# Kernel optimization log

Measured on AMD Instinct MI355X. Metric: run time of the kernel, lower is better.

## Reference

```python
import jax, jax.numpy as jnp
import numpy as np

E, K = 8, 2              # n_routed_experts, num_experts_per_tok
H, I = 2048, 1408        # hidden_size, moe_intermediate_size
IS = 2 * I               # shared experts intermediate (n_shared_experts * I)
B, S = 2, 512


def setup_inputs() -> dict:
    key = jax.random.key(0)
    ks = jax.random.split(key, 8)
    w = 0.02
    return {
        "hidden_states": jax.random.normal(ks[0], (B, S, H), jnp.float32),
        "router_w": jax.random.normal(ks[1], (E, H), jnp.float32) * w,
        "w_gate": jax.random.normal(ks[2], (E, I, H), jnp.float32) * w,
        "w_up": jax.random.normal(ks[3], (E, I, H), jnp.float32) * w,
        "w_down": jax.random.normal(ks[4], (E, H, I), jnp.float32) * w,
        "sw_gate": jax.random.normal(ks[5], (IS, H), jnp.float32) * w,
        "sw_up": jax.random.normal(ks[6], (IS, H), jnp.float32) * w,
        "sw_down": jax.random.normal(ks[7], (H, IS), jnp.float32) * w,
    }


def reference(hidden_states, router_w, w_gate, w_up, w_down, sw_gate, sw_up, sw_down):
    b, s, h = hidden_states.shape
    x = hidden_states.reshape(-1, h)                      # [T, H]
    t = x.shape[0]

    # Router: F.linear(x, gate_weight) -> softmax (fp32) -> topk (sorted)
    router_logits = x @ router_w.T                        # [T, E]
    scores = jax.nn.softmax(router_logits.astype(jnp.float32), axis=-1)
    routing_weights, selected = jax.lax.top_k(scores, K)  # [T, K]
    routing_weights = routing_weights / (routing_weights.sum(-1, keepdims=True) + 1e-6)
    routing_weights = routing_weights.astype(x.dtype)

    # Combine weights: [T, E], zero where expert not selected (exact gather/scatter math)
    cw = jnp.zeros((t, E), x.dtype).at[jnp.arange(t)[:, None], selected].add(routing_weights)

    # Per-expert SwiGLU FFN, batched over experts (grouped GEMM form)
    g = jnp.einsum('td,eid->eti', x, w_gate)              # [E, T, I]
    u = jnp.einsum('td,eid->eti', x, w_up)                # [E, T, I]
    y = jnp.einsum('eti,edi->etd', jax.nn.silu(g) * u, w_down)  # [E, T, H]
    moe_out = jnp.einsum('etd,te->td', y, cw)             # weighted combine -> [T, H]

    # Shared experts SwiGLU over all tokens
    shared = (jax.nn.silu(x @ sw_gate.T) * (x @ sw_up.T)) @ sw_down.T  # [T, H]

    final = (moe_out + shared).reshape(b, s, h)
    return final, router_logits
```

## Files before the change

### kernel.cpp

```cpp
#include <hip/hip_runtime.h>
#include <hip/hip_bf16.h>
#include <math.h>

#define T_TOK 1024
#define HDIM  2048
#define NEXP  8
#define IDIM  1408
#define ISH   2816
#define ROW_CAP 3072
#define ROWS_ALL 4096
#define MOE_TILES 24
#define NT_TOT 32

typedef __attribute__((ext_vector_type(8))) short bf16x8;
typedef __attribute__((ext_vector_type(4))) float f32x4;

static __device__ __forceinline__ unsigned short f2bf(float f) {
  __hip_bfloat16 h = __float2bfloat16(f);
  return __builtin_bit_cast(unsigned short, h);
}

__global__ __launch_bounds__(256) void router_kernel(
    const float* __restrict__ x, const float* __restrict__ rw,
    float* __restrict__ logits_out, int* __restrict__ selk, float* __restrict__ cwk)
{
  int t = blockIdx.x;
  int tid = threadIdx.x;
  float part[NEXP];
  const float* xr = x + (size_t)t * HDIM + tid * 8;
  float4 xa = *reinterpret_cast<const float4*>(xr);
  float4 xb = *reinterpret_cast<const float4*>(xr + 4);
  for (int e = 0; e < NEXP; ++e) {
    const float* wp = rw + (size_t)e * HDIM + tid * 8;
    float4 wa = *reinterpret_cast<const float4*>(wp);
    float4 wb = *reinterpret_cast<const float4*>(wp + 4);
    part[e] = xa.x*wa.x + xa.y*wa.y + xa.z*wa.z + xa.w*wa.w
            + xb.x*wb.x + xb.y*wb.y + xb.z*wb.z + xb.w*wb.w;
  }
  for (int e = 0; e < NEXP; ++e)
    for (int off = 32; off; off >>= 1)
      part[e] += __shfl_xor(part[e], off, 64);
  __shared__ float sums[4][NEXP];
  int wid = tid >> 6, lane = tid & 63;
  if (lane == 0) for (int e = 0; e < NEXP; ++e) sums[wid][e] = part[e];
  __syncthreads();
  if (tid == 0) {
    float lg[NEXP];
    for (int e = 0; e < NEXP; ++e) lg[e] = sums[0][e] + sums[1][e] + sums[2][e] + sums[3][e];
    float mx = lg[0];
    for (int e = 1; e < NEXP; ++e) mx = fmaxf(mx, lg[e]);
    float p[NEXP], s = 0.f;
    for (int e = 0; e < NEXP; ++e) { p[e] = expf(lg[e] - mx); s += p[e]; }
    for (int e = 0; e < NEXP; ++e) p[e] /= s;
    int i1 = 0;
    for (int e = 1; e < NEXP; ++e) if (lg[e] > lg[i1]) i1 = e;
    int i2 = -1;
    for (int e = 0; e < NEXP; ++e) { if (e == i1) continue; if (i2 < 0 || lg[e] > lg[i2]) i2 = e; }
    float denom = p[i1] + p[i2] + 1e-6f;
    selk[t*2] = i1; selk[t*2+1] = i2;
    cwk[t*2] = p[i1] / denom; cwk[t*2+1] = p[i2] / denom;
    for (int e = 0; e < NEXP; ++e) logits_out[t * NEXP + e] = lg[e];
  }
}

__global__ __launch_bounds__(512) void plan_kernel(
    const int* __restrict__ selk, const float* __restrict__ cwk,
    int* __restrict__ rowidx, int* __restrict__ tok_of_row,
    float* __restrict__ rowwgt, int* __restrict__ tile_tab)
{
  __shared__ int cnt[NEXP];
  __shared__ int seg[NEXP];
  int tid = threadIdx.x;
  int w = tid >> 6, lane = tid & 63;
  for (int i = tid; i < ROW_CAP; i += 512) { tok_of_row[i] = -1; rowwgt[i] = 0.f; }
  for (int i = tid; i < T_TOK; i += 512) { tok_of_row[ROW_CAP + i] = i; rowwgt[ROW_CAP + i] = 1.f; }
  int total = 0;
  for (int base = 0; base < 2 * T_TOK; base += 64) {
    unsigned long long m = __ballot(selk[base + lane] == w);
    total += __popcll(m);
  }
  if (lane == 0) cnt[w] = total;
  __syncthreads();
  if (tid == 0) {
    int s = 0;
    for (int e = 0; e < NEXP; ++e) { seg[e] = s; s += (cnt[e] + 127) & ~127; }
  }
  __syncthreads();
  int run = seg[w];
  for (int base = 0; base < 2 * T_TOK; base += 64) {
    int i = base + lane;
    bool f = selk[i] == w;
    unsigned long long m = __ballot(f);
    if (f) {
      int r = run + __popcll(m & ((1ull << lane) - 1ull));
      rowidx[i] = r;
      tok_of_row[r] = i >> 1;
      rowwgt[r] = cwk[i];
    }
    run += __popcll(m);
  }
  __syncthreads();
  if (tid < NT_TOT) {
    int e = -1, valid = 0;
    if (tid < MOE_TILES) {
      int base = tid * 128;
      for (int k = 0; k < NEXP; ++k) {
        int s0 = seg[k], s1 = s0 + ((cnt[k] + 127) & ~127);
        if (base >= s0 && base < s1) {
          e = k;
          valid = cnt[k] - (base - s0);
          if (valid > 128) valid = 128;
          if (valid < 0) valid = 0;
        }
      }
    } else { e = 0; valid = 128; }
    tile_tab[tid*2] = e;
    tile_tab[tid*2+1] = valid;
  }
}

__global__ __launch_bounds__(256) void gather_kernel(
    const float* __restrict__ x, const int* __restrict__ tok_of_row,
    unsigned short* __restrict__ xg)
{
  int r = blockIdx.x;
  int tid = threadIdx.x;
  int tok = tok_of_row[r];
  unsigned short* dst = xg + (size_t)r * HDIM + tid * 8;
  union { unsigned short us[8]; uint4 q; } p;
  if (tok < 0) {
    p.q = uint4{0, 0, 0, 0};
  } else {
    const float* src = x + (size_t)tok * HDIM + tid * 8;
    float4 a = *reinterpret_cast<const float4*>(src);
    float4 b = *reinterpret_cast<const float4*>(src + 4);
    p.us[0]=f2bf(a.x); p.us[1]=f2bf(a.y); p.us[2]=f2bf(a.z); p.us[3]=f2bf(a.w);
    p.us[4]=f2bf(b.x); p.us[5]=f2bf(b.y); p.us[6]=f2bf(b.z); p.us[7]=f2bf(b.w);
  }
  *reinterpret_cast<uint4*>(dst) = p.q;
}

static __device__ __forceinline__ void stage_b(
    const float* __restrict__ src, unsigned short (*Bs)[72], int brow, int bc)
{
  float4 v0 = *reinterpret_cast<const float4*>(src);
  float4 v1 = *reinterpret_cast<const float4*>(src + 4);
  float4 v2 = *reinterpret_cast<const float4*>(src + 8);
  float4 v3 = *reinterpret_cast<const float4*>(src + 12);
  union { unsigned short us[8]; uint4 q; } a, b;
  a.us[0]=f2bf(v0.x); a.us[1]=f2bf(v0.y); a.us[2]=f2bf(v0.z); a.us[3]=f2bf(v0.w);
  a.us[4]=f2bf(v1.x); a.us[5]=f2bf(v1.y); a.us[6]=f2bf(v1.z); a.us[7]=f2bf(v1.w);
  b.us[0]=f2bf(v2.x); b.us[1]=f2bf(v2.y); b.us[2]=f2bf(v2.z); b.us[3]=f2bf(v2.w);
  b.us[4]=f2bf(v3.x); b.us[5]=f2bf(v3.y); b.us[6]=f2bf(v3.z); b.us[7]=f2bf(v3.w);
  *reinterpret_cast<uint4*>(&Bs[brow][bc]) = a.q;
  *reinterpret_cast<uint4*>(&Bs[brow][bc + 8]) = b.q;
}

static __device__ __forceinline__ void stage_a(
    const unsigned short* __restrict__ abase, size_t lda, int k0,
    unsigned short* As, int wid, int lane)
{
  #pragma unroll
  for (int j = 0; j < 2; ++j) {
    int row = j * 64 + wid * 8 + (lane >> 3);
    int col = ((lane & 7) ^ (row & 7)) << 3;
    const unsigned short* src = abase + (size_t)row * lda + k0 + col;
    unsigned short* dst = &As[(j * 64 + wid * 8) * 64];
    __builtin_amdgcn_global_load_lds(
        (const __attribute__((address_space(1))) void*)src,
        (__attribute__((address_space(3))) void*)dst, 16, 0, 0);
  }
}

__global__ __launch_bounds__(512) void gu_kernel(
    const unsigned short* __restrict__ xg,
    const float* __restrict__ w_gate, const float* __restrict__ w_up,
    const float* __restrict__ sw_gate, const float* __restrict__ sw_up,
    const float* __restrict__ rowwgt, const int* __restrict__ tile_tab,
    unsigned short* __restrict__ hg, unsigned short* __restrict__ hsh)
{
  int mt = blockIdx.y, nt = blockIdx.x;
  int e = tile_tab[mt*2], valid = tile_tab[mt*2+1];
  bool sh = mt >= MOE_TILES;
  int ntiles = sh ? (ISH / 128) : (IDIM / 128);
  if (valid <= 0 || nt >= ntiles) return;
  int m0 = mt * 128, n0 = nt * 128;
  const float *wg, *wu; unsigned short* hout; int ldo;
  if (sh) { wg = sw_gate; wu = sw_up; hout = hsh + (size_t)(m0 - ROW_CAP) * ISH; ldo = ISH; }
  else {
    size_t wo = (size_t)e * IDIM * HDIM;
    wg = w_gate + wo; wu = w_up + wo;
    hout = hg + (size_t)m0 * IDIM; ldo = IDIM;
  }

  __shared__ unsigned short As[128 * 64];
  __shared__ unsigned short BgS[128][72];
  __shared__ unsigned short BuS[128][72];

  int tid = threadIdx.x, wid = tid >> 6, lane = tid & 63;
  int wr = wid >> 2, wc = wid & 3;
  int fr = lane & 15, fq8 = (lane >> 4) << 3;

  f32x4 accg[4][2] = {{}};
  f32x4 accu[4][2] = {{}};

  int brow = tid >> 2, bc = (tid & 3) << 4;
  const float* gsrc = wg + (size_t)(n0 + brow) * HDIM + bc;
  const float* usrc = wu + (size_t)(n0 + brow) * HDIM + bc;
  const unsigned short* abase = xg + (size_t)m0 * HDIM;

  for (int k0 = 0; k0 < HDIM; k0 += 64) {
    stage_a(abase, HDIM, k0, As, wid, lane);
    stage_b(gsrc + k0, BgS, brow, bc);
    stage_b(usrc + k0, BuS, brow, bc);
    __syncthreads();
    #pragma unroll
    for (int kk = 0; kk < 64; kk += 32) {
      bf16x8 a[4], bg[2], bu[2];
      #pragma unroll
      for (int m = 0; m < 4; ++m) {
        int row = wr * 64 + m * 16 + fr;
        a[m] = *reinterpret_cast<const bf16x8*>(&As[row * 64 + ((kk + fq8) ^ ((row & 7) << 3))]);
      }
      #pragma unroll
      for (int n = 0; n < 2; ++n) {
        bg[n] = *reinterpret_cast<const bf16x8*>(&BgS[wc * 32 + n * 16 + fr][kk + fq8]);
        bu[n] = *reinterpret_cast<const bf16x8*>(&BuS[wc * 32 + n * 16 + fr][kk + fq8]);
      }
      #pragma unroll
      for (int m = 0; m < 4; ++m)
        #pragma unroll
        for (int n = 0; n < 2; ++n) {
          accg[m][n] = __builtin_amdgcn_mfma_f32_16x16x32_bf16(a[m], bg[n], accg[m][n], 0, 0, 0);
          accu[m][n] = __builtin_amdgcn_mfma_f32_16x16x32_bf16(a[m], bu[n], accu[m][n], 0, 0, 0);
        }
    }
    __syncthreads();
  }
  int fq = lane >> 4;
  #pragma unroll
  for (int m = 0; m < 4; ++m)
    #pragma unroll
    for (int j = 0; j < 4; ++j) {
      int grow = wr * 64 + m * 16 + fq * 4 + j;
      float wv = rowwgt[m0 + grow];
      #pragma unroll
      for (int n = 0; n < 2; ++n) {
        float g = accg[m][n][j], u = accu[m][n][j];
        float hv = g / (1.f + __expf(-g)) * u * wv;
        hout[(size_t)grow * ldo + n0 + wc * 32 + n * 16 + fr] = f2bf(hv);
      }
    }
}

__global__ __launch_bounds__(512) void dn_kernel(
    const unsigned short* __restrict__ hg, const unsigned short* __restrict__ hsh,
    const float* __restrict__ w_down, const float* __restrict__ sw_down,
    const int* __restrict__ tile_tab,
    float* __restrict__ ydn, float* __restrict__ outf)
{
  int mt = blockIdx.y, nt = blockIdx.x;
  int e = tile_tab[mt*2], valid = tile_tab[mt*2+1];
  bool sh = mt >= MOE_TILES;
  if (valid <= 0) return;
  int m0 = mt * 128, n0 = nt * 128;
  const unsigned short* abase; const float* bbase; int K; float* obase;
  if (sh) { abase = hsh + (size_t)(m0 - ROW_CAP) * ISH; K = ISH; bbase = sw_down; obase = outf + (size_t)(m0 - ROW_CAP) * HDIM; }
  else { abase = hg + (size_t)m0 * IDIM; K = IDIM; bbase = w_down + (size_t)e * HDIM * IDIM; obase = ydn + (size_t)m0 * HDIM; }

  __shared__ unsigned short As[128 * 64];
  __shared__ unsigned short BsS[128][72];

  int tid = threadIdx.x, wid = tid >> 6, lane = tid & 63;
  int wr = wid >> 2, wc = wid & 3;
  int fr = lane & 15, fq8 = (lane >> 4) << 3;

  f32x4 acc[4][2] = {{}};

  int brow = tid >> 2, bc = (tid & 3) << 4;
  const float* bsrc = bbase + (size_t)(n0 + brow) * K + bc;

  for (int k0 = 0; k0 < K; k0 += 64) {
    stage_a(abase, K, k0, As, wid, lane);
    stage_b(bsrc + k0, BsS, brow, bc);
    __syncthreads();
    #pragma unroll
    for (int kk = 0; kk < 64; kk += 32) {
      bf16x8 a[4], b[2];
      #pragma unroll
      for (int m = 0; m < 4; ++m) {
        int row = wr * 64 + m * 16 + fr;
        a[m] = *reinterpret_cast<const bf16x8*>(&As[row * 64 + ((kk + fq8) ^ ((row & 7) << 3))]);
      }
      #pragma unroll
      for (int n = 0; n < 2; ++n)
        b[n] = *reinterpret_cast<const bf16x8*>(&BsS[wc * 32 + n * 16 + fr][kk + fq8]);
      #pragma unroll
      for (int m = 0; m < 4; ++m)
        #pragma unroll
        for (int n = 0; n < 2; ++n)
          acc[m][n] = __builtin_amdgcn_mfma_f32_16x16x32_bf16(a[m], b[n], acc[m][n], 0, 0, 0);
    }
    __syncthreads();
  }
  int fq = lane >> 4;
  #pragma unroll
  for (int m = 0; m < 4; ++m)
    #pragma unroll
    for (int j = 0; j < 4; ++j) {
      int grow = wr * 64 + m * 16 + fq * 4 + j;
      #pragma unroll
      for (int n = 0; n < 2; ++n)
        obase[(size_t)grow * HDIM + n0 + wc * 32 + n * 16 + fr] = acc[m][n][j];
    }
}

__global__ __launch_bounds__(256) void combine_kernel(
    const float* __restrict__ ydn, const int* __restrict__ rowidx,
    float* __restrict__ outf)
{
  int t = blockIdx.x;
  int c = threadIdx.x * 8;
  int r0 = rowidx[t*2], r1 = rowidx[t*2+1];
  const float4* a0 = reinterpret_cast<const float4*>(ydn + (size_t)r0 * HDIM + c);
  const float4* a1 = reinterpret_cast<const float4*>(ydn + (size_t)r1 * HDIM + c);
  float4* o = reinterpret_cast<float4*>(outf + (size_t)t * HDIM + c);
  float4 x0 = a0[0], x1 = a0[1], y0 = a1[0], y1 = a1[1];
  float4 o0 = o[0], o1 = o[1];
  o0.x += x0.x + y0.x; o0.y += x0.y + y0.y; o0.z += x0.z + y0.z; o0.w += x0.w + y0.w;
  o1.x += x1.x + y1.x; o1.y += x1.y + y1.y; o1.z += x1.z + y1.z; o1.w += x1.w + y1.w;
  o[0] = o0; o[1] = o1;
}

extern "C" void kernel_launch(void* const* d_in, const int* in_sizes, int n_in,
                              void* d_out, int out_size, void* d_ws, size_t ws_size,
                              hipStream_t stream) {
  const float* x      = (const float*)d_in[0];
  const float* rw     = (const float*)d_in[1];
  const float* w_gate = (const float*)d_in[2];
  const float* w_up   = (const float*)d_in[3];
  const float* w_down = (const float*)d_in[4];
  const float* sw_g   = (const float*)d_in[5];
  const float* sw_u   = (const float*)d_in[6];
  const float* sw_d   = (const float*)d_in[7];
  float* out_final  = (float*)d_out;
  float* out_logits = out_final + (size_t)T_TOK * HDIM;

  char* ws = (char*)d_ws;
  int*   selk     = (int*)(ws + 0);
  float* cwk      = (float*)(ws + 8192);
  int*   rowidx   = (int*)(ws + 16384);
  int*   tokrow   = (int*)(ws + 24576);
  float* rowwgt   = (float*)(ws + 40960);
  int*   tile_tab = (int*)(ws + 57344);
  unsigned short* xg  = (unsigned short*)(ws + 65536);
  unsigned short* hg  = (unsigned short*)(ws + 65536 + 16777216);
  unsigned short* hsh = (unsigned short*)(ws + 65536 + 16777216 + 8650752);
  float* ydn = (float*)(ws + 65536 + 16777216 + 8650752 + 5767168);

  router_kernel<<<T_TOK, 256, 0, stream>>>(x, rw, out_logits, selk, cwk);
  plan_kernel<<<1, 512, 0, stream>>>(selk, cwk, rowidx, tokrow, rowwgt, tile_tab);
  gather_kernel<<<ROWS_ALL, 256, 0, stream>>>(x, tokrow, xg);
  gu_kernel<<<dim3(ISH / 128, NT_TOT), 512, 0, stream>>>(
      xg, w_gate, w_up, sw_g, sw_u, rowwgt, tile_tab, hg, hsh);
  dn_kernel<<<dim3(HDIM / 128, NT_TOT), 512, 0, stream>>>(
      hg, hsh, w_down, sw_d, tile_tab, ydn, out_final);
  combine_kernel<<<T_TOK, 256, 0, stream>>>(ydn, rowidx, out_final);
}
```

Before: 276.5 us.

## Software-pipeline GEMM K-loop with double-buffered A and remap tile launch order

Both grouped GEMM kernels now prefetch the next K-slice: the A tile goes asynchronously into a second LDS buffer, and the fp32 weight slice is loaded into registers while the current slice's MFMAs run. The register copy is converted and written to LDS after a barrier. The 2D grid is replaced by a flat 1D grid with a custom block-to-tile mapping. This drops the dead blocks the old grid spent on MoE tiles with too few column tiles, and interleaves blocks across the XCDs so weight tiles are shared. The cost is more registers and LDS, and an extra barrier per iteration.

```diff
diff --git a/kernel.cpp b/kernel.cpp
--- a/kernel.cpp
+++ b/kernel.cpp
@@ -140,20 +140,24 @@
   *reinterpret_cast<uint4*>(dst) = p.q;
 }
 
-static __device__ __forceinline__ void stage_b(
-    const float* __restrict__ src, unsigned short (*Bs)[72], int brow, int bc)
-{
-  float4 v0 = *reinterpret_cast<const float4*>(src);
-  float4 v1 = *reinterpret_cast<const float4*>(src + 4);
-  float4 v2 = *reinterpret_cast<const float4*>(src + 8);
-  float4 v3 = *reinterpret_cast<const float4*>(src + 12);
+static __device__ __forceinline__ void bwrite(
+    unsigned short (*Bs)[72], int brow, int bc, const float4* v)
+{
   union { unsigned short us[8]; uint4 q; } a, b;
-  a.us[0]=f2bf(v0.x); a.us[1]=f2bf(v0.y); a.us[2]=f2bf(v0.z); a.us[3]=f2bf(v0.w);
-  a.us[4]=f2bf(v1.x); a.us[5]=f2bf(v1.y); a.us[6]=f2bf(v1.z); a.us[7]=f2bf(v1.w);
-  b.us[0]=f2bf(v2.x); b.us[1]=f2bf(v2.y); b.us[2]=f2bf(v2.z); b.us[3]=f2bf(v2.w);
-  b.us[4]=f2bf(v3.x); b.us[5]=f2bf(v3.y); b.us[6]=f2bf(v3.z); b.us[7]=f2bf(v3.w);
+  a.us[0]=f2bf(v[0].x); a.us[1]=f2bf(v[0].y); a.us[2]=f2bf(v[0].z); a.us[3]=f2bf(v[0].w);
+  a.us[4]=f2bf(v[1].x); a.us[5]=f2bf(v[1].y); a.us[6]=f2bf(v[1].z); a.us[7]=f2bf(v[1].w);
+  b.us[0]=f2bf(v[2].x); b.us[1]=f2bf(v[2].y); b.us[2]=f2bf(v[2].z); b.us[3]=f2bf(v[2].w);
+  b.us[4]=f2bf(v[3].x); b.us[5]=f2bf(v[3].y); b.us[6]=f2bf(v[3].z); b.us[7]=f2bf(v[3].w);
   *reinterpret_cast<uint4*>(&Bs[brow][bc]) = a.q;
   *reinterpret_cast<uint4*>(&Bs[brow][bc + 8]) = b.q;
+}
+
+static __device__ __forceinline__ void bload(const float* __restrict__ src, float4* v)
+{
+  v[0] = *reinterpret_cast<const float4*>(src);
+  v[1] = *reinterpret_cast<const float4*>(src + 4);
+  v[2] = *reinterpret_cast<const float4*>(src + 8);
+  v[3] = *reinterpret_cast<const float4*>(src + 12);
 }
 
 static __device__ __forceinline__ void stage_a(
@@ -179,11 +183,15 @@
     const float* __restrict__ rowwgt, const int* __restrict__ tile_tab,
     unsigned short* __restrict__ hg, unsigned short* __restrict__ hsh)
 {
-  int mt = blockIdx.y, nt = blockIdx.x;
+  int bid = blockIdx.x;
+  int lb = (bid & 7) * 55 + (bid >> 3);
+  int mt, nt;
+  if (lb < MOE_TILES * 11) { mt = lb % MOE_TILES; nt = lb / MOE_TILES; }
+  else { int s = lb - MOE_TILES * 11; mt = MOE_TILES + (s & 7); nt = s >> 3; }
+
   int e = tile_tab[mt*2], valid = tile_tab[mt*2+1];
+  if (valid <= 0) return;
   bool sh = mt >= MOE_TILES;
-  int ntiles = sh ? (ISH / 128) : (IDIM / 128);
-  if (valid <= 0 || nt >= ntiles) return;
   int m0 = mt * 128, n0 = nt * 128;
   const float *wg, *wu; unsigned short* hout; int ldo;
   if (sh) { wg = sw_gate; wu = sw_up; hout = hsh + (size_t)(m0 - ROW_CAP) * ISH; ldo = ISH; }
@@ -193,7 +201,7 @@
     hout = hg + (size_t)m0 * IDIM; ldo = IDIM;
   }
 
-  __shared__ unsigned short As[128 * 64];
+  __shared__ unsigned short As[2][128 * 64];
   __shared__ unsigned short BgS[128][72];
   __shared__ unsigned short BuS[128][72];
 
@@ -209,18 +217,26 @@
   const float* usrc = wu + (size_t)(n0 + brow) * HDIM + bc;
   const unsigned short* abase = xg + (size_t)m0 * HDIM;
 
-  for (int k0 = 0; k0 < HDIM; k0 += 64) {
-    stage_a(abase, HDIM, k0, As, wid, lane);
-    stage_b(gsrc + k0, BgS, brow, bc);
-    stage_b(usrc + k0, BuS, brow, bc);
-    __syncthreads();
+  float4 pg[4], pu[4];
+  bload(gsrc, pg); bload(usrc, pu);
+  stage_a(abase, HDIM, 0, As[0], wid, lane);
+  bwrite(BgS, brow, bc, pg);
+  bwrite(BuS, brow, bc, pu);
+  __syncthreads();
+
+  const int NK = HDIM / 64;
+  for (int t = 0; t < NK; ++t) {
+    int cur = t & 1;
+    int k1 = (t + 1 < NK) ? (t + 1) * 64 : 0;
+    bload(gsrc + k1, pg); bload(usrc + k1, pu);
+    stage_a(abase, HDIM, k1, As[cur ^ 1], wid, lane);
     #pragma unroll
     for (int kk = 0; kk < 64; kk += 32) {
       bf16x8 a[4], bg[2], bu[2];
       #pragma unroll
       for (int m = 0; m < 4; ++m) {
         int row = wr * 64 + m * 16 + fr;
-        a[m] = *reinterpret_cast<const bf16x8*>(&As[row * 64 + ((kk + fq8) ^ ((row & 7) << 3))]);
+        a[m] = *reinterpret_cast<const bf16x8*>(&As[cur][row * 64 + ((kk + fq8) ^ ((row & 7) << 3))]);
       }
       #pragma unroll
       for (int n = 0; n < 2; ++n) {
@@ -236,7 +252,11 @@
         }
     }
     __syncthreads();
-  }
+    bwrite(BgS, brow, bc, pg);
+    bwrite(BuS, brow, bc, pu);
+    __syncthreads();
+  }
+
   int fq = lane >> 4;
   #pragma unroll
   for (int m = 0; m < 4; ++m)
@@ -259,16 +279,21 @@
     const int* __restrict__ tile_tab,
     float* __restrict__ ydn, float* __restrict__ outf)
 {
-  int mt = blockIdx.y, nt = blockIdx.x;
+  int bid = blockIdx.x;
+  int lb = (bid & 7) * 64 + (bid >> 3);
+  int mt, nt;
+  if (lb < MOE_TILES * 16) { mt = lb % MOE_TILES; nt = lb / MOE_TILES; }
+  else { int s = lb - MOE_TILES * 16; mt = MOE_TILES + (s & 7); nt = s >> 3; }
+
   int e = tile_tab[mt*2], valid = tile_tab[mt*2+1];
+  if (valid <= 0) return;
   bool sh = mt >= MOE_TILES;
-  if (valid <= 0) return;
   int m0 = mt * 128, n0 = nt * 128;
   const unsigned short* abase; const float* bbase; int K; float* obase;
   if (sh) { abase = hsh + (size_t)(m0 - ROW_CAP) * ISH; K = ISH; bbase = sw_down; obase = outf + (size_t)(m0 - ROW_CAP) * HDIM; }
   else { abase = hg + (size_t)m0 * IDIM; K = IDIM; bbase = w_down + (size_t)e * HDIM * IDIM; obase = ydn + (size_t)m0 * HDIM; }
 
-  __shared__ unsigned short As[128 * 64];
+  __shared__ unsigned short As[2][128 * 64];
   __shared__ unsigned short BsS[128][72];
 
   int tid = threadIdx.x, wid = tid >> 6, lane = tid & 63;
@@ -280,17 +305,25 @@
   int brow = tid >> 2, bc = (tid & 3) << 4;
   const float* bsrc = bbase + (size_t)(n0 + brow) * K + bc;
 
-  for (int k0 = 0; k0 < K; k0 += 64) {
-    stage_a(abase, K, k0, As, wid, lane);
-    stage_b(bsrc + k0, BsS, brow, bc);
-    __syncthreads();
+  float4 pb[4];
+  bload(bsrc, pb);
+  stage_a(abase, K, 0, As[0], wid, lane);
+  bwrite(BsS, brow, bc, pb);
+  __syncthreads();
+
+  const int NK = K / 64;
+  for (int t = 0; t < NK; ++t) {
+    int cur = t & 1;
+    int k1 = (t + 1 < NK) ? (t + 1) * 64 : 0;
+    bload(bsrc + k1, pb);
+    stage_a(abase, K, k1, As[cur ^ 1], wid, lane);
     #pragma unroll
     for (int kk = 0; kk < 64; kk += 32) {
       bf16x8 a[4], b[2];
       #pragma unroll
       for (int m = 0; m < 4; ++m) {
         int row = wr * 64 + m * 16 + fr;
-        a[m] = *reinterpret_cast<const bf16x8*>(&As[row * 64 + ((kk + fq8) ^ ((row & 7) << 3))]);
+        a[m] = *reinterpret_cast<const bf16x8*>(&As[cur][row * 64 + ((kk + fq8) ^ ((row & 7) << 3))]);
       }
       #pragma unroll
       for (int n = 0; n < 2; ++n)
@@ -301,6 +334,8 @@
         for (int n = 0; n < 2; ++n)
           acc[m][n] = __builtin_amdgcn_mfma_f32_16x16x32_bf16(a[m], b[n], acc[m][n], 0, 0, 0);
     }
+    __syncthreads();
+    bwrite(BsS, brow, bc, pb);
     __syncthreads();
   }
   int fq = lane >> 4;
@@ -361,9 +396,9 @@
   router_kernel<<<T_TOK, 256, 0, stream>>>(x, rw, out_logits, selk, cwk);
   plan_kernel<<<1, 512, 0, stream>>>(selk, cwk, rowidx, tokrow, rowwgt, tile_tab);
   gather_kernel<<<ROWS_ALL, 256, 0, stream>>>(x, tokrow, xg);
-  gu_kernel<<<dim3(ISH / 128, NT_TOT), 512, 0, stream>>>(
+  gu_kernel<<<440, 512, 0, stream>>>(
       xg, w_gate, w_up, sw_g, sw_u, rowwgt, tile_tab, hg, hsh);
-  dn_kernel<<<dim3(HDIM / 128, NT_TOT), 512, 0, stream>>>(
+  dn_kernel<<<512, 512, 0, stream>>>(
       hg, hsh, w_down, sw_d, tile_tab, ydn, out_final);
   combine_kernel<<<T_TOK, 256, 0, stream>>>(ydn, rowidx, out_final);
 }
```

Result: slower. 338.8 us (+22.5%).

## Restructure MoE GEMMs into 128x32 tiles with triple-buffered A and register-direct B

Applied to the files above, without the earlier changes.

The gate/up and down GEMM kernels now use 128x32 output tiles with 256 threads. B weights are loaded straight from global fp32 into registers and converted to bf16 in-register, which drops the LDS staging for B. The A operand is triple-buffered in LDS via global_load_lds, and a vmcnt-based wait plus one barrier per step replaces the two __syncthreads. The 1D grid is remapped with an XCD-aware (bid&7) swizzle that groups tiles sharing weight columns. This aims to overlap loads with MFMA and raise parallelism, but each block re-reads A for fewer output columns and the hand-tuned vmcnt counts are fragile.

```diff
diff --git a/kernel.cpp b/kernel.cpp
--- a/kernel.cpp
+++ b/kernel.cpp
@@ -11,6 +11,7 @@
 #define ROWS_ALL 4096
 #define MOE_TILES 24
 #define NT_TOT 32
+#define ATILE (128*64)
 
 typedef __attribute__((ext_vector_type(8))) short bf16x8;
 typedef __attribute__((ext_vector_type(4))) float f32x4;
@@ -18,6 +19,13 @@
 static __device__ __forceinline__ unsigned short f2bf(float f) {
   __hip_bfloat16 h = __float2bfloat16(f);
   return __builtin_bit_cast(unsigned short, h);
+}
+
+static __device__ __forceinline__ bf16x8 cvt8(float4 a, float4 b) {
+  union { unsigned short us[8]; bf16x8 v; } r;
+  r.us[0]=f2bf(a.x); r.us[1]=f2bf(a.y); r.us[2]=f2bf(a.z); r.us[3]=f2bf(a.w);
+  r.us[4]=f2bf(b.x); r.us[5]=f2bf(b.y); r.us[6]=f2bf(b.z); r.us[7]=f2bf(b.w);
+  return r.v;
 }
 
 __global__ __launch_bounds__(256) void router_kernel(
@@ -140,51 +148,116 @@
   *reinterpret_cast<uint4*>(dst) = p.q;
 }
 
-static __device__ __forceinline__ void stage_b(
-    const float* __restrict__ src, unsigned short (*Bs)[72], int brow, int bc)
-{
-  float4 v0 = *reinterpret_cast<const float4*>(src);
-  float4 v1 = *reinterpret_cast<const float4*>(src + 4);
-  float4 v2 = *reinterpret_cast<const float4*>(src + 8);
-  float4 v3 = *reinterpret_cast<const float4*>(src + 12);
-  union { unsigned short us[8]; uint4 q; } a, b;
-  a.us[0]=f2bf(v0.x); a.us[1]=f2bf(v0.y); a.us[2]=f2bf(v0.z); a.us[3]=f2bf(v0.w);
-  a.us[4]=f2bf(v1.x); a.us[5]=f2bf(v1.y); a.us[6]=f2bf(v1.z); a.us[7]=f2bf(v1.w);
-  b.us[0]=f2bf(v2.x); b.us[1]=f2bf(v2.y); b.us[2]=f2bf(v2.z); b.us[3]=f2bf(v2.w);
-  b.us[4]=f2bf(v3.x); b.us[5]=f2bf(v3.y); b.us[6]=f2bf(v3.z); b.us[7]=f2bf(v3.w);
-  *reinterpret_cast<uint4*>(&Bs[brow][bc]) = a.q;
-  *reinterpret_cast<uint4*>(&Bs[brow][bc + 8]) = b.q;
-}
-
-static __device__ __forceinline__ void stage_a(
+static __device__ __forceinline__ void stage_a3(
     const unsigned short* __restrict__ abase, size_t lda, int k0,
     unsigned short* As, int wid, int lane)
 {
   #pragma unroll
-  for (int j = 0; j < 2; ++j) {
-    int row = j * 64 + wid * 8 + (lane >> 3);
+  for (int j = 0; j < 4; ++j) {
+    int row = j * 32 + wid * 8 + (lane >> 3);
     int col = ((lane & 7) ^ (row & 7)) << 3;
     const unsigned short* src = abase + (size_t)row * lda + k0 + col;
-    unsigned short* dst = &As[(j * 64 + wid * 8) * 64];
+    unsigned short* dst = &As[(j * 32 + wid * 8) * 64];
     __builtin_amdgcn_global_load_lds(
         (const __attribute__((address_space(1))) void*)src,
         (__attribute__((address_space(3))) void*)dst, 16, 0, 0);
   }
 }
 
-__global__ __launch_bounds__(512) void gu_kernel(
+struct BStage2 { float4 g0, g1, g2, g3, u0, u1, u2, u3; };
+struct BStage1 { float4 b0, b1, b2, b3; };
+
+static __device__ __forceinline__ void loadB2(
+    const float* __restrict__ pg, const float* __restrict__ pu, int k, BStage2& s)
+{
+  s.g0 = *reinterpret_cast<const float4*>(pg + k);
+  s.g1 = *reinterpret_cast<const float4*>(pg + k + 4);
+  s.g2 = *reinterpret_cast<const float4*>(pg + k + 32);
+  s.g3 = *reinterpret_cast<const float4*>(pg + k + 36);
+  s.u0 = *reinterpret_cast<const float4*>(pu + k);
+  s.u1 = *reinterpret_cast<const float4*>(pu + k + 4);
+  s.u2 = *reinterpret_cast<const float4*>(pu + k + 32);
+  s.u3 = *reinterpret_cast<const float4*>(pu + k + 36);
+}
+
+static __device__ __forceinline__ void loadB1(
+    const float* __restrict__ pb, int k, BStage1& s)
+{
+  s.b0 = *reinterpret_cast<const float4*>(pb + k);
+  s.b1 = *reinterpret_cast<const float4*>(pb + k + 4);
+  s.b2 = *reinterpret_cast<const float4*>(pb + k + 32);
+  s.b3 = *reinterpret_cast<const float4*>(pb + k + 36);
+}
+
+static __device__ __forceinline__ void stepGU(
+    const BStage2& s, const unsigned short* Abuf,
+    int wr, int fr, int fq8, f32x4* accg, f32x4* accu)
+{
+  bf16x8 bg0 = cvt8(s.g0, s.g1), bg1 = cvt8(s.g2, s.g3);
+  bf16x8 bu0 = cvt8(s.u0, s.u1), bu1 = cvt8(s.u2, s.u3);
+  #pragma unroll
+  for (int kk = 0; kk < 2; ++kk) {
+    bf16x8 a[4];
+    #pragma unroll
+    for (int m = 0; m < 4; ++m) {
+      int row = wr * 64 + m * 16 + fr;
+      a[m] = *reinterpret_cast<const bf16x8*>(
+          &Abuf[row * 64 + ((kk * 32 + fq8) ^ ((row & 7) << 3))]);
+    }
+    bf16x8 bg = kk ? bg1 : bg0;
+    bf16x8 bu = kk ? bu1 : bu0;
+    #pragma unroll
+    for (int m = 0; m < 4; ++m) {
+      accg[m] = __builtin_amdgcn_mfma_f32_16x16x32_bf16(a[m], bg, accg[m], 0, 0, 0);
+      accu[m] = __builtin_amdgcn_mfma_f32_16x16x32_bf16(a[m], bu, accu[m], 0, 0, 0);
+    }
+  }
+}
+
+static __device__ __forceinline__ void stepDN(
+    const BStage1& s, const unsigned short* Abuf,
+    int wr, int fr, int fq8, f32x4* acc)
+{
+  bf16x8 b0 = cvt8(s.b0, s.b1), b1 = cvt8(s.b2, s.b3);
+  #pragma unroll
+  for (int kk = 0; kk < 2; ++kk) {
+    bf16x8 a[4];
+    #pragma unroll
+    for (int m = 0; m < 4; ++m) {
+      int row = wr * 64 + m * 16 + fr;
+      a[m] = *reinterpret_cast<const bf16x8*>(
+          &Abuf[row * 64 + ((kk * 32 + fq8) ^ ((row & 7) << 3))]);
+    }
+    bf16x8 b = kk ? b1 : b0;
+    #pragma unroll
+    for (int m = 0; m < 4; ++m)
+      acc[m] = __builtin_amdgcn_mfma_f32_16x16x32_bf16(a[m], b, acc[m], 0, 0, 0);
+  }
+}
+
+#define WAIT_BARRIER(N) do { \
+    asm volatile("s_waitcnt vmcnt(" #N ")" ::: "memory"); \
+    __builtin_amdgcn_s_barrier(); \
+    __builtin_amdgcn_sched_barrier(0); \
+  } while (0)
+
+__global__ __launch_bounds__(256) void gu_kernel(
     const unsigned short* __restrict__ xg,
     const float* __restrict__ w_gate, const float* __restrict__ w_up,
     const float* __restrict__ sw_gate, const float* __restrict__ sw_up,
     const float* __restrict__ rowwgt, const int* __restrict__ tile_tab,
     unsigned short* __restrict__ hg, unsigned short* __restrict__ hsh)
 {
-  int mt = blockIdx.y, nt = blockIdx.x;
+  int bid = blockIdx.x;
+  int lb = (bid & 7) * 220 + (bid >> 3);
+  int mt, nt;
+  if (lb < MOE_TILES * 44) { mt = lb % MOE_TILES; nt = lb / MOE_TILES; }
+  else { int s = lb - MOE_TILES * 44; mt = MOE_TILES + (s & 7); nt = s >> 3; }
+
   int e = tile_tab[mt*2], valid = tile_tab[mt*2+1];
+  if (valid <= 0) return;
   bool sh = mt >= MOE_TILES;
-  int ntiles = sh ? (ISH / 128) : (IDIM / 128);
-  if (valid <= 0 || nt >= ntiles) return;
-  int m0 = mt * 128, n0 = nt * 128;
+  int m0 = mt * 128, n0 = nt * 32;
   const float *wg, *wu; unsigned short* hout; int ldo;
   if (sh) { wg = sw_gate; wu = sw_up; hout = hsh + (size_t)(m0 - ROW_CAP) * ISH; ldo = ISH; }
   else {
@@ -193,50 +266,45 @@
     hout = hg + (size_t)m0 * IDIM; ldo = IDIM;
   }
 
-  __shared__ unsigned short As[128 * 64];
-  __shared__ unsigned short BgS[128][72];
-  __shared__ unsigned short BuS[128][72];
+  __shared__ unsigned short As[3 * ATILE];
 
   int tid = threadIdx.x, wid = tid >> 6, lane = tid & 63;
-  int wr = wid >> 2, wc = wid & 3;
+  int wr = wid >> 1, wc = wid & 1;
   int fr = lane & 15, fq8 = (lane >> 4) << 3;
 
-  f32x4 accg[4][2] = {{}};
-  f32x4 accu[4][2] = {{}};
-
-  int brow = tid >> 2, bc = (tid & 3) << 4;
-  const float* gsrc = wg + (size_t)(n0 + brow) * HDIM + bc;
-  const float* usrc = wu + (size_t)(n0 + brow) * HDIM + bc;
+  f32x4 accg[4] = {};
+  f32x4 accu[4] = {};
+
+  int col = n0 + wc * 16 + fr;
+  const float* pg_ = wg + (size_t)col * HDIM + fq8;
+  const float* pu_ = wu + (size_t)col * HDIM + fq8;
   const unsigned short* abase = xg + (size_t)m0 * HDIM;
 
-  for (int k0 = 0; k0 < HDIM; k0 += 64) {
-    stage_a(abase, HDIM, k0, As, wid, lane);
-    stage_b(gsrc + k0, BgS, brow, bc);
-    stage_b(usrc + k0, BuS, brow, bc);
-    __syncthreads();
-    #pragma unroll
-    for (int kk = 0; kk < 64; kk += 32) {
-      bf16x8 a[4], bg[2], bu[2];
-      #pragma unroll
-      for (int m = 0; m < 4; ++m) {
-        int row = wr * 64 + m * 16 + fr;
-        a[m] = *reinterpret_cast<const bf16x8*>(&As[row * 64 + ((kk + fq8) ^ ((row & 7) << 3))]);
-      }
-      #pragma unroll
-      for (int n = 0; n < 2; ++n) {
-        bg[n] = *reinterpret_cast<const bf16x8*>(&BgS[wc * 32 + n * 16 + fr][kk + fq8]);
-        bu[n] = *reinterpret_cast<const bf16x8*>(&BuS[wc * 32 + n * 16 + fr][kk + fq8]);
-      }
-      #pragma unroll
-      for (int m = 0; m < 4; ++m)
-        #pragma unroll
-        for (int n = 0; n < 2; ++n) {
-          accg[m][n] = __builtin_amdgcn_mfma_f32_16x16x32_bf16(a[m], bg[n], accg[m][n], 0, 0, 0);
-          accu[m][n] = __builtin_amdgcn_mfma_f32_16x16x32_bf16(a[m], bu[n], accu[m][n], 0, 0, 0);
-        }
-    }
-    __syncthreads();
-  }
+  BStage2 st0, st1;
+  stage_a3(abase, HDIM, 0, As, wid, lane);
+  loadB2(pg_, pu_, 0, st0);
+
+  int use = 0, fill = 1;
+  const int NK = HDIM / 64;
+  for (int t = 0; t < NK; t += 2) {
+    {
+      int k1 = (t + 1 < NK) ? (t + 1) * 64 : 0;
+      stage_a3(abase, HDIM, k1, As + fill * ATILE, wid, lane);
+      loadB2(pg_, pu_, k1, st1);
+      WAIT_BARRIER(12);
+      stepGU(st0, As + use * ATILE, wr, fr, fq8, accg, accu);
+      int nu = fill, nf = 3 - use - fill; use = nu; fill = nf;
+    }
+    {
+      int k1 = (t + 2 < NK) ? (t + 2) * 64 : 0;
+      stage_a3(abase, HDIM, k1, As + fill * ATILE, wid, lane);
+      loadB2(pg_, pu_, k1, st0);
+      WAIT_BARRIER(12);
+      stepGU(st1, As + use * ATILE, wr, fr, fq8, accg, accu);
+      int nu = fill, nf = 3 - use - fill; use = nu; fill = nf;
+    }
+  }
+
   int fq = lane >> 4;
   #pragma unroll
   for (int m = 0; m < 4; ++m)
@@ -244,74 +312,75 @@
     for (int j = 0; j < 4; ++j) {
       int grow = wr * 64 + m * 16 + fq * 4 + j;
       float wv = rowwgt[m0 + grow];
-      #pragma unroll
-      for (int n = 0; n < 2; ++n) {
-        float g = accg[m][n][j], u = accu[m][n][j];
-        float hv = g / (1.f + __expf(-g)) * u * wv;
-        hout[(size_t)grow * ldo + n0 + wc * 32 + n * 16 + fr] = f2bf(hv);
-      }
-    }
-}
-
-__global__ __launch_bounds__(512) void dn_kernel(
+      float g = accg[m][j], u = accu[m][j];
+      float hv = g / (1.f + __expf(-g)) * u * wv;
+      hout[(size_t)grow * ldo + col] = f2bf(hv);
+    }
+}
+
+__global__ __launch_bounds__(256) void dn_kernel(
     const unsigned short* __restrict__ hg, const unsigned short* __restrict__ hsh,
     const float* __restrict__ w_down, const float* __restrict__ sw_down,
     const int* __restrict__ tile_tab,
     float* __restrict__ ydn, float* __restrict__ outf)
 {
-  int mt = blockIdx.y, nt = blockIdx.x;
+  int bid = blockIdx.x;
+  int lb = (bid & 7) * 256 + (bid >> 3);
+  int mt, nt;
+  if (lb < MOE_TILES * 64) { mt = lb % MOE_TILES; nt = lb / MOE_TILES; }
+  else { int s = lb - MOE_TILES * 64; mt = MOE_TILES + (s & 7); nt = s >> 3; }
+
   int e = tile_tab[mt*2], valid = tile_tab[mt*2+1];
+  if (valid <= 0) return;
   bool sh = mt >= MOE_TILES;
-  if (valid <= 0) return;
-  int m0 = mt * 128, n0 = nt * 128;
+  int m0 = mt * 128, n0 = nt * 32;
   const unsigned short* abase; const float* bbase; int K; float* obase;
   if (sh) { abase = hsh + (size_t)(m0 - ROW_CAP) * ISH; K = ISH; bbase = sw_down; obase = outf + (size_t)(m0 - ROW_CAP) * HDIM; }
   else { abase = hg + (size_t)m0 * IDIM; K = IDIM; bbase = w_down + (size_t)e * HDIM * IDIM; obase = ydn + (size_t)m0 * HDIM; }
 
-  __shared__ unsigned short As[128 * 64];
-  __shared__ unsigned short BsS[128][72];
+  __shared__ unsigned short As[3 * ATILE];
 
   int tid = threadIdx.x, wid = tid >> 6, lane = tid & 63;
-  int wr = wid >> 2, wc = wid & 3;
+  int wr = wid >> 1, wc = wid & 1;
   int fr = lane & 15, fq8 = (lane >> 4) << 3;
 
-  f32x4 acc[4][2] = {{}};
-
-  int brow = tid >> 2, bc = (tid & 3) << 4;
-  const float* bsrc = bbase + (size_t)(n0 + brow) * K + bc;
-
-  for (int k0 = 0; k0 < K; k0 += 64) {
-    stage_a(abase, K, k0, As, wid, lane);
-    stage_b(bsrc + k0, BsS, brow, bc);
-    __syncthreads();
-    #pragma unroll
-    for (int kk = 0; kk < 64; kk += 32) {
-      bf16x8 a[4], b[2];
-      #pragma unroll
-      for (int m = 0; m < 4; ++m) {
-        int row = wr * 64 + m * 16 + fr;
-        a[m] = *reinterpret_cast<const bf16x8*>(&As[row * 64 + ((kk + fq8) ^ ((row & 7) << 3))]);
-      }
-      #pragma unroll
-      for (int n = 0; n < 2; ++n)
-        b[n] = *reinterpret_cast<const bf16x8*>(&BsS[wc * 32 + n * 16 + fr][kk + fq8]);
-      #pragma unroll
-      for (int m = 0; m < 4; ++m)
-        #pragma unroll
-        for (int n = 0; n < 2; ++n)
-          acc[m][n] = __builtin_amdgcn_mfma_f32_16x16x32_bf16(a[m], b[n], acc[m][n], 0, 0, 0);
-    }
-    __syncthreads();
-  }
+  f32x4 acc[4] = {};
+
+  int col = n0 + wc * 16 + fr;
+  const float* pb_ = bbase + (size_t)col * K + fq8;
+
+  BStage1 st0, st1;
+  stage_a3(abase, K, 0, As, wid, lane);
+  loadB1(pb_, 0, st0);
+
+  int use = 0, fill = 1;
+  const int NK = K / 64;
+  for (int t = 0; t < NK; t += 2) {
+    {
+      int k1 = (t + 1 < NK) ? (t + 1) * 64 : 0;
+      stage_a3(abase, K, k1, As + fill * ATILE, wid, lane);
+      loadB1(pb_, k1, st1);
+      WAIT_BARRIER(8);
+      stepDN(st0, As + use * ATILE, wr, fr, fq8, acc);
+      int nu = fill, nf = 3 - use - fill; use = nu; fill = nf;
+    }
+    {
+      int k1 = (t + 2 < NK) ? (t + 2) * 64 : 0;
+      stage_a3(abase, K, k1, As + fill * ATILE, wid, lane);
+      loadB1(pb_, k1, st0);
+      WAIT_BARRIER(8);
+      stepDN(st1, As + use * ATILE, wr, fr, fq8, acc);
+      int nu = fill, nf = 3 - use - fill; use = nu; fill = nf;
+    }
+  }
+
   int fq = lane >> 4;
   #pragma unroll
   for (int m = 0; m < 4; ++m)
     #pragma unroll
     for (int j = 0; j < 4; ++j) {
       int grow = wr * 64 + m * 16 + fq * 4 + j;
-      #pragma unroll
-      for (int n = 0; n < 2; ++n)
-        obase[(size_t)grow * HDIM + n0 + wc * 32 + n * 16 + fr] = acc[m][n][j];
+      obase[(size_t)grow * HDIM + col] = acc[m][j];
     }
 }
 
@@ -361,9 +430,9 @@
   router_kernel<<<T_TOK, 256, 0, stream>>>(x, rw, out_logits, selk, cwk);
   plan_kernel<<<1, 512, 0, stream>>>(selk, cwk, rowidx, tokrow, rowwgt, tile_tab);
   gather_kernel<<<ROWS_ALL, 256, 0, stream>>>(x, tokrow, xg);
-  gu_kernel<<<dim3(ISH / 128, NT_TOT), 512, 0, stream>>>(
+  gu_kernel<<<1760, 256, 0, stream>>>(
       xg, w_gate, w_up, sw_g, sw_u, rowwgt, tile_tab, hg, hsh);
-  dn_kernel<<<dim3(HDIM / 128, NT_TOT), 512, 0, stream>>>(
+  dn_kernel<<<2048, 256, 0, stream>>>(
       hg, hsh, w_down, sw_d, tile_tab, ydn, out_final);
   combine_kernel<<<T_TOK, 256, 0, stream>>>(ydn, rowidx, out_final);
 }
```

After: 532.8 us. 1.93x slower.

## Stage fp32 weights directly into LDS asynchronously and shrink tiles to 128x64

Applied to the files above, without the earlier changes.

Weight tiles are now copied as raw fp32 straight from global memory into swizzled LDS with global_load_lds. Conversion to bf16 moves to fragment load time, replacing the old path that loaded through registers and converted before the LDS store. Tiles shrink from 128x128 to 128x64 with 256-thread blocks and an occupancy hint of 3, doubling the grid. The aim is to overlap weight traffic asynchronously and raise occupancy, at the cost of more LDS bytes per weight element and repeated conversion work per fragment read.

```diff
diff --git a/kernel.cpp b/kernel.cpp
--- a/kernel.cpp
+++ b/kernel.cpp
@@ -140,39 +140,54 @@
   *reinterpret_cast<uint4*>(dst) = p.q;
 }
 
-static __device__ __forceinline__ void stage_b(
-    const float* __restrict__ src, unsigned short (*Bs)[72], int brow, int bc)
-{
-  float4 v0 = *reinterpret_cast<const float4*>(src);
-  float4 v1 = *reinterpret_cast<const float4*>(src + 4);
-  float4 v2 = *reinterpret_cast<const float4*>(src + 8);
-  float4 v3 = *reinterpret_cast<const float4*>(src + 12);
-  union { unsigned short us[8]; uint4 q; } a, b;
-  a.us[0]=f2bf(v0.x); a.us[1]=f2bf(v0.y); a.us[2]=f2bf(v0.z); a.us[3]=f2bf(v0.w);
-  a.us[4]=f2bf(v1.x); a.us[5]=f2bf(v1.y); a.us[6]=f2bf(v1.z); a.us[7]=f2bf(v1.w);
-  b.us[0]=f2bf(v2.x); b.us[1]=f2bf(v2.y); b.us[2]=f2bf(v2.z); b.us[3]=f2bf(v2.w);
-  b.us[4]=f2bf(v3.x); b.us[5]=f2bf(v3.y); b.us[6]=f2bf(v3.z); b.us[7]=f2bf(v3.w);
-  *reinterpret_cast<uint4*>(&Bs[brow][bc]) = a.q;
-  *reinterpret_cast<uint4*>(&Bs[brow][bc + 8]) = b.q;
-}
-
-static __device__ __forceinline__ void stage_a(
+static __device__ __forceinline__ void stage_a4(
     const unsigned short* __restrict__ abase, size_t lda, int k0,
     unsigned short* As, int wid, int lane)
 {
   #pragma unroll
-  for (int j = 0; j < 2; ++j) {
-    int row = j * 64 + wid * 8 + (lane >> 3);
+  for (int j = 0; j < 4; ++j) {
+    int row = j * 32 + wid * 8 + (lane >> 3);
     int col = ((lane & 7) ^ (row & 7)) << 3;
     const unsigned short* src = abase + (size_t)row * lda + k0 + col;
-    unsigned short* dst = &As[(j * 64 + wid * 8) * 64];
+    unsigned short* dst = &As[(j * 32 + wid * 8) * 64];
     __builtin_amdgcn_global_load_lds(
         (const __attribute__((address_space(1))) void*)src,
         (__attribute__((address_space(3))) void*)dst, 16, 0, 0);
   }
 }
 
-__global__ __launch_bounds__(512) void gu_kernel(
+static __device__ __forceinline__ void stage_bf32(
+    const float* __restrict__ bbase, size_t ldb, int k0,
+    float* Bf, int wid, int lane)
+{
+  int c16 = lane & 15;
+  #pragma unroll
+  for (int j = 0; j < 4; ++j) {
+    int rl = j * 16 + wid * 4 + (lane >> 4);
+    int X  = (rl & 7) ^ ((rl & 8) >> 1);
+    int sc = ((((c16 >> 1) ^ X) << 1) | (c16 & 1)) << 2;
+    const float* src = bbase + (size_t)rl * ldb + k0 + sc;
+    float* dst = &Bf[(j * 16 + wid * 4) * 64];
+    __builtin_amdgcn_global_load_lds(
+        (const __attribute__((address_space(1))) void*)src,
+        (__attribute__((address_space(3))) void*)dst, 16, 0, 0);
+  }
+}
+
+static __device__ __forceinline__ bf16x8 ldb_frag(
+    const float* Bf, int rl, int kk, int kq)
+{
+  int X = (rl & 7) ^ ((rl & 8) >> 1);
+  int s = ((kk << 2) + kq) ^ X;
+  const float4* p = reinterpret_cast<const float4*>(Bf + rl * 64 + s * 8);
+  float4 q0 = p[0], q1 = p[1];
+  union { unsigned short us[8]; bf16x8 v; } r;
+  r.us[0]=f2bf(q0.x); r.us[1]=f2bf(q0.y); r.us[2]=f2bf(q0.z); r.us[3]=f2bf(q0.w);
+  r.us[4]=f2bf(q1.x); r.us[5]=f2bf(q1.y); r.us[6]=f2bf(q1.z); r.us[7]=f2bf(q1.w);
+  return r.v;
+}
+
+__global__ __launch_bounds__(256, 3) void gu_kernel(
     const unsigned short* __restrict__ xg,
     const float* __restrict__ w_gate, const float* __restrict__ w_up,
     const float* __restrict__ sw_gate, const float* __restrict__ sw_up,
@@ -182,9 +197,9 @@
   int mt = blockIdx.y, nt = blockIdx.x;
   int e = tile_tab[mt*2], valid = tile_tab[mt*2+1];
   bool sh = mt >= MOE_TILES;
-  int ntiles = sh ? (ISH / 128) : (IDIM / 128);
+  int ntiles = sh ? (ISH / 64) : (IDIM / 64);
   if (valid <= 0 || nt >= ntiles) return;
-  int m0 = mt * 128, n0 = nt * 128;
+  int m0 = mt * 128, n0 = nt * 64;
   const float *wg, *wu; unsigned short* hout; int ldo;
   if (sh) { wg = sw_gate; wu = sw_up; hout = hsh + (size_t)(m0 - ROW_CAP) * ISH; ldo = ISH; }
   else {
@@ -194,38 +209,39 @@
   }
 
   __shared__ unsigned short As[128 * 64];
-  __shared__ unsigned short BgS[128][72];
-  __shared__ unsigned short BuS[128][72];
+  __shared__ float BgF[64 * 64];
+  __shared__ float BuF[64 * 64];
 
   int tid = threadIdx.x, wid = tid >> 6, lane = tid & 63;
-  int wr = wid >> 2, wc = wid & 3;
-  int fr = lane & 15, fq8 = (lane >> 4) << 3;
+  int wr = wid >> 1, wc = wid & 1;
+  int fr = lane & 15, fq = lane >> 4, fq8 = fq << 3;
 
   f32x4 accg[4][2] = {{}};
   f32x4 accu[4][2] = {{}};
 
-  int brow = tid >> 2, bc = (tid & 3) << 4;
-  const float* gsrc = wg + (size_t)(n0 + brow) * HDIM + bc;
-  const float* usrc = wu + (size_t)(n0 + brow) * HDIM + bc;
+  const float* gsrc = wg + (size_t)n0 * HDIM;
+  const float* usrc = wu + (size_t)n0 * HDIM;
   const unsigned short* abase = xg + (size_t)m0 * HDIM;
 
   for (int k0 = 0; k0 < HDIM; k0 += 64) {
-    stage_a(abase, HDIM, k0, As, wid, lane);
-    stage_b(gsrc + k0, BgS, brow, bc);
-    stage_b(usrc + k0, BuS, brow, bc);
+    stage_a4(abase, HDIM, k0, As, wid, lane);
+    stage_bf32(gsrc, HDIM, k0, BgF, wid, lane);
+    stage_bf32(usrc, HDIM, k0, BuF, wid, lane);
     __syncthreads();
     #pragma unroll
-    for (int kk = 0; kk < 64; kk += 32) {
+    for (int kk = 0; kk < 2; ++kk) {
       bf16x8 a[4], bg[2], bu[2];
       #pragma unroll
       for (int m = 0; m < 4; ++m) {
         int row = wr * 64 + m * 16 + fr;
-        a[m] = *reinterpret_cast<const bf16x8*>(&As[row * 64 + ((kk + fq8) ^ ((row & 7) << 3))]);
+        a[m] = *reinterpret_cast<const bf16x8*>(
+            &As[row * 64 + ((kk * 32 + fq8) ^ ((row & 7) << 3))]);
       }
       #pragma unroll
       for (int n = 0; n < 2; ++n) {
-        bg[n] = *reinterpret_cast<const bf16x8*>(&BgS[wc * 32 + n * 16 + fr][kk + fq8]);
-        bu[n] = *reinterpret_cast<const bf16x8*>(&BuS[wc * 32 + n * 16 + fr][kk + fq8]);
+        int rl = wc * 32 + n * 16 + fr;
+        bg[n] = ldb_frag(BgF, rl, kk, fq);
+        bu[n] = ldb_frag(BuF, rl, kk, fq);
       }
       #pragma unroll
       for (int m = 0; m < 4; ++m)
@@ -237,7 +253,7 @@
     }
     __syncthreads();
   }
-  int fq = lane >> 4;
+
   #pragma unroll
   for (int m = 0; m < 4; ++m)
     #pragma unroll
@@ -253,7 +269,7 @@
     }
 }
 
-__global__ __launch_bounds__(512) void dn_kernel(
+__global__ __launch_bounds__(256, 3) void dn_kernel(
     const unsigned short* __restrict__ hg, const unsigned short* __restrict__ hsh,
     const float* __restrict__ w_down, const float* __restrict__ sw_down,
     const int* __restrict__ tile_tab,
@@ -261,40 +277,40 @@
 {
   int mt = blockIdx.y, nt = blockIdx.x;
   int e = tile_tab[mt*2], valid = tile_tab[mt*2+1];
+  if (valid <= 0) return;
   bool sh = mt >= MOE_TILES;
-  if (valid <= 0) return;
-  int m0 = mt * 128, n0 = nt * 128;
+  int m0 = mt * 128, n0 = nt * 64;
   const unsigned short* abase; const float* bbase; int K; float* obase;
   if (sh) { abase = hsh + (size_t)(m0 - ROW_CAP) * ISH; K = ISH; bbase = sw_down; obase = outf + (size_t)(m0 - ROW_CAP) * HDIM; }
   else { abase = hg + (size_t)m0 * IDIM; K = IDIM; bbase = w_down + (size_t)e * HDIM * IDIM; obase = ydn + (size_t)m0 * HDIM; }
 
   __shared__ unsigned short As[128 * 64];
-  __shared__ unsigned short BsS[128][72];
+  __shared__ float BsF[64 * 64];
 
   int tid = threadIdx.x, wid = tid >> 6, lane = tid & 63;
-  int wr = wid >> 2, wc = wid & 3;
-  int fr = lane & 15, fq8 = (lane >> 4) << 3;
+  int wr = wid >> 1, wc = wid & 1;
+  int fr = lane & 15, fq = lane >> 4, fq8 = fq << 3;
 
   f32x4 acc[4][2] = {{}};
 
-  int brow = tid >> 2, bc = (tid & 3) << 4;
-  const float* bsrc = bbase + (size_t)(n0 + brow) * K + bc;
+  const float* bsrc = bbase + (size_t)n0 * K;
 
   for (int k0 = 0; k0 < K; k0 += 64) {
-    stage_a(abase, K, k0, As, wid, lane);
-    stage_b(bsrc + k0, BsS, brow, bc);
+    stage_a4(abase, K, k0, As, wid, lane);
+    stage_bf32(bsrc, K, k0, BsF, wid, lane);
     __syncthreads();
     #pragma unroll
-    for (int kk = 0; kk < 64; kk += 32) {
+    for (int kk = 0; kk < 2; ++kk) {
       bf16x8 a[4], b[2];
       #pragma unroll
       for (int m = 0; m < 4; ++m) {
         int row = wr * 64 + m * 16 + fr;
-        a[m] = *reinterpret_cast<const bf16x8*>(&As[row * 64 + ((kk + fq8) ^ ((row & 7) << 3))]);
+        a[m] = *reinterpret_cast<const bf16x8*>(
+            &As[row * 64 + ((kk * 32 + fq8) ^ ((row & 7) << 3))]);
       }
       #pragma unroll
       for (int n = 0; n < 2; ++n)
-        b[n] = *reinterpret_cast<const bf16x8*>(&BsS[wc * 32 + n * 16 + fr][kk + fq8]);
+        b[n] = ldb_frag(BsF, wc * 32 + n * 16 + fr, kk, fq);
       #pragma unroll
       for (int m = 0; m < 4; ++m)
         #pragma unroll
@@ -303,7 +319,6 @@
     }
     __syncthreads();
   }
-  int fq = lane >> 4;
   #pragma unroll
   for (int m = 0; m < 4; ++m)
     #pragma unroll
@@ -361,9 +376,9 @@
   router_kernel<<<T_TOK, 256, 0, stream>>>(x, rw, out_logits, selk, cwk);
   plan_kernel<<<1, 512, 0, stream>>>(selk, cwk, rowidx, tokrow, rowwgt, tile_tab);
   gather_kernel<<<ROWS_ALL, 256, 0, stream>>>(x, tokrow, xg);
-  gu_kernel<<<dim3(ISH / 128, NT_TOT), 512, 0, stream>>>(
+  gu_kernel<<<dim3(ISH / 64, NT_TOT), 256, 0, stream>>>(
       xg, w_gate, w_up, sw_g, sw_u, rowwgt, tile_tab, hg, hsh);
-  dn_kernel<<<dim3(HDIM / 128, NT_TOT), 512, 0, stream>>>(
+  dn_kernel<<<dim3(HDIM / 64, NT_TOT), 256, 0, stream>>>(
       hg, hsh, w_down, sw_d, tile_tab, ydn, out_final);
   combine_kernel<<<T_TOK, 256, 0, stream>>>(ydn, rowidx, out_final);
 }
```

Result: slower. 389.4 us (+40.8%).
